# Optimization experiments

Hardware: AMD Instinct MI355X
Metric: run time of the kernel (lower is better)

Reference implementation:

```python
import jax, jax.numpy as jnp
import numpy as np
from jax import lax

B, C, H, W = 2, 128, 128, 128
Hs, Ws = 64, 64
DG, KK = 8, 9          # deformable groups, kernel positions (3x3)
CG = C // DG           # channels per deformable group = 16
COUT = C // 2          # dcn output channels = 64


def setup_inputs() -> dict:
    key = jax.random.key(0)
    ks = jax.random.split(key, 9)
    s = 0.05
    return {
        "feat_l": jax.random.normal(ks[0], (B, C, H, W), jnp.float32),
        "feat_s": jax.random.normal(ks[1], (B, C, Hs, Ws), jnp.float32),
        "fsm_w": jax.random.normal(ks[2], (C, C, 1, 1), jnp.float32) * s,
        "offset_w": jax.random.normal(ks[3], (C, 2 * C, 1, 1), jnp.float32) * s,
        "com_w": jax.random.normal(ks[4], (3 * DG * KK, C, 3, 3), jnp.float32) * s,
        "com_b": jax.random.normal(ks[5], (3 * DG * KK,), jnp.float32) * s,
        "dcn_w": jax.random.normal(ks[6], (COUT, C, 3, 3), jnp.float32) * s,
        "dcn_b": jax.random.normal(ks[7], (COUT,), jnp.float32) * s,
        "cat_w": jax.random.normal(ks[8], (C, COUT, 1, 1), jnp.float32) * s,
    }


def _conv(x, w, pad):
    return lax.conv_general_dilated(x, w, (1, 1), [(pad, pad), (pad, pad)],
                                    dimension_numbers=("NCHW", "OIHW", "NCHW"))


def _bilinear(feat_g, py, px):
    # feat_g: [B,DG,CG,H,W]; py/px: [B,DG,KK,H,W] fractional sample coords.
    Hf, Wf = feat_g.shape[-2], feat_g.shape[-1]
    y0 = jnp.floor(py)
    x0 = jnp.floor(px)
    ly = py - y0
    lx = px - x0
    y0i = y0.astype(jnp.int32)
    x0i = x0.astype(jnp.int32)
    flat = feat_g.reshape(B, DG, 1, CG, Hf * Wf)  # broadcast over KK

    def gather(yi, xi, wgt):
        valid = ((yi >= 0) & (yi < Hf) & (xi >= 0) & (xi < Wf)).astype(feat_g.dtype)
        idx = (jnp.clip(yi, 0, Hf - 1) * Wf + jnp.clip(xi, 0, Wf - 1))
        idx = idx.reshape(B, DG, KK, 1, H * W)
        v = jnp.take_along_axis(flat, idx, axis=-1)  # [B,DG,KK,CG,H*W]
        return v * (wgt * valid).reshape(B, DG, KK, 1, H * W)

    acc = (gather(y0i, x0i, (1 - ly) * (1 - lx))
           + gather(y0i, x0i + 1, (1 - ly) * lx)
           + gather(y0i + 1, x0i, ly * (1 - lx))
           + gather(y0i + 1, x0i + 1, ly * lx))
    return acc.reshape(B, DG, KK, CG, H, W)


def reference(feat_l, feat_s, fsm_w, offset_w, com_w, com_b, dcn_w, dcn_b, cat_w):
    # nearest-neighbor upsample of feat_s to feat_l's HxW (F.interpolate nearest)
    idx_h = (jnp.arange(H) * Hs) // H
    idx_w = (jnp.arange(W) * Ws) // W
    feat_up = feat_s[:, :, idx_h][:, :, :, idx_w]

    feat_arm = jax.nn.relu(_conv(feat_l, fsm_w, 0))                       # FSM (1x1 conv+relu)
    off_feat = jax.nn.relu(_conv(jnp.concatenate([feat_arm, feat_up * 2], axis=1), offset_w, 0))

    # DCNv2 pack: 3x3 conv -> (o1, o2, mask)
    om = _conv(off_feat, com_w, 1) + com_b[None, :, None, None]
    o1, o2, m = jnp.split(om, 3, axis=1)
    offset = jnp.concatenate([o1, o2], axis=1).reshape(B, DG, KK, 2, H, W)  # (y,x) per (g,pos)
    mask = jax.nn.sigmoid(m).reshape(B, DG, KK, H, W)

    # sampling coords: p + kernel offset + learned offset (stride=1, pad=1, dil=1)
    kyy = (jnp.arange(KK) // 3 - 1).astype(jnp.float32)
    kxx = (jnp.arange(KK) % 3 - 1).astype(jnp.float32)
    py = (jnp.arange(H, dtype=jnp.float32)[None, None, None, :, None]
          + kyy[None, None, :, None, None] + offset[:, :, :, 0])
    px = (jnp.arange(W, dtype=jnp.float32)[None, None, None, None, :]
          + kxx[None, None, :, None, None] + offset[:, :, :, 1])

    feat_g = feat_up.reshape(B, DG, CG, H, W)
    val = _bilinear(feat_g, py, px) * mask[:, :, :, None]  # [B,DG,KK,CG,H,W]

    w_r = dcn_w.reshape(COUT, DG, CG, KK)
    out = jnp.einsum('bgkchw,ogck->bohw', val, w_r) + dcn_b[None, :, None, None]
    feat_align = jax.nn.relu(out)

    return jax.nn.relu(_conv(feat_align, cat_w, 0)) + feat_arm
```

## Files before the change

kernel.cpp:

```cpp
#include <hip/hip_runtime.h>
#include <cstdint>
#include <cstddef>


typedef _Float16 f16x8 __attribute__((ext_vector_type(8)));
typedef _Float16 f16x4 __attribute__((ext_vector_type(4)));
typedef float    f32x4 __attribute__((ext_vector_type(4)));

__device__ __forceinline__ float relu_(float x) { return fmaxf(x, 0.f); }

template<int MODE, int CIN>
__global__ __launch_bounds__(256) void conv1x1_kernel(
    const float* __restrict__ in1, const float* __restrict__ in2,
    const float* __restrict__ Wm, float* __restrict__ out)
{
  constexpr int IN1C = (MODE == 2) ? 64 : 128;
  const int b  = blockIdx.y;
  const int p0 = blockIdx.x * 64;
  const int tid = threadIdx.x;
  const int tx = tid & 7;
  const int ty = tid >> 3;

  __shared__ float Xs[16][64];
  __shared__ float Wt[16][128];

  float acc[4][8];
#pragma unroll
  for (int i = 0; i < 4; ++i)
#pragma unroll
    for (int j = 0; j < 8; ++j) acc[i][j] = 0.f;

  const int cS  = tid >> 4;
  const int pxS = (tid & 15) * 4;
  const int ocS = (tid & 15) * 8;

  for (int cc = 0; cc < CIN; cc += 16) {
    __syncthreads();
    {
      int gc = cc + cS;
      float4 v;
      if (MODE == 1 && gc >= 128) {
        int sc = gc - 128;
        float t[4];
#pragma unroll
        for (int j = 0; j < 4; ++j) {
          int pp = p0 + pxS + j;
          int hh = pp >> 7, ww = pp & 127;
          t[j] = 2.f * in2[((size_t)(b * 128 + sc) << 12) + ((hh >> 1) << 6) + (ww >> 1)];
        }
        v = make_float4(t[0], t[1], t[2], t[3]);
      } else {
        v = *(const float4*)(in1 + ((size_t)(b * IN1C + gc) << 14) + p0 + pxS);
      }
      *(float4*)&Xs[cS][pxS] = v;
#pragma unroll
      for (int j = 0; j < 8; ++j)
        Wt[cS][ocS + j] = Wm[(ocS + j) * CIN + cc + cS];
    }
    __syncthreads();
#pragma unroll
    for (int c = 0; c < 16; ++c) {
      float4 wv = *(const float4*)&Wt[c][ty * 4];
      float4 x0 = *(const float4*)&Xs[c][tx * 8];
      float4 x1 = *(const float4*)&Xs[c][tx * 8 + 4];
      float xs[8] = {x0.x, x0.y, x0.z, x0.w, x1.x, x1.y, x1.z, x1.w};
      float wf[4] = {wv.x, wv.y, wv.z, wv.w};
#pragma unroll
      for (int i = 0; i < 4; ++i)
#pragma unroll
        for (int j = 0; j < 8; ++j)
          acc[i][j] = fmaf(wf[i], xs[j], acc[i][j]);
    }
  }

#pragma unroll
  for (int i = 0; i < 4; ++i) {
    int oc = ty * 4 + i;
    size_t base = ((size_t)(b * 128 + oc) << 14) + p0 + tx * 8;
    float r[8];
#pragma unroll
    for (int j = 0; j < 8; ++j) r[j] = relu_(acc[i][j]);
    if (MODE == 2) {
#pragma unroll
      for (int j = 0; j < 8; ++j) r[j] += in2[base + j];
    }
    *(float4*)(out + base)     = make_float4(r[0], r[1], r[2], r[3]);
    *(float4*)(out + base + 4) = make_float4(r[4], r[5], r[6], r[7]);
  }
}

__global__ __launch_bounds__(256) void t2h_kernel(
    const float* __restrict__ src, _Float16* __restrict__ dst, int HW)
{
  const int b  = blockIdx.z;
  const int c0 = blockIdx.y * 32;
  const int p0 = blockIdx.x * 32;
  const int tid = threadIdx.x;
  __shared__ float T[32][33];
  {
    int pxl = tid & 31, cy = tid >> 5;
#pragma unroll
    for (int j = 0; j < 4; ++j) {
      int c = cy + j * 8;
      T[c][pxl] = src[((size_t)(b * 128 + c0 + c)) * HW + p0 + pxl];
    }
  }
  __syncthreads();
  {
    int cq = tid & 7, pr = tid >> 3;
    f16x4 v;
#pragma unroll
    for (int e = 0; e < 4; ++e) v[e] = (_Float16)T[cq * 4 + e][pr];
    *(f16x4*)&dst[(((size_t)b * HW) + p0 + pr) * 128 + c0 + cq * 4] = v;
  }
}

__global__ __launch_bounds__(256) void wfA_kernel(
    const float* __restrict__ w, _Float16* __restrict__ Wf)
{
  int idx = blockIdx.x * 256 + threadIdx.x;
  int lane = idx & 63;
  int t = idx >> 6;
  int m = t & 7, q = t >> 3;
  int oc = m * 16 + (lane & 15);
  int c0 = q * 32 + (lane >> 4) * 8;
  f16x8 v;
#pragma unroll
  for (int j = 0; j < 8; ++j) v[j] = (_Float16)w[oc * 128 + c0 + j];
  ((f16x8*)Wf)[idx] = v;
}

__global__ __launch_bounds__(256) void wfB_kernel(
    const float* __restrict__ w, _Float16* __restrict__ Wf)
{
  int idx = blockIdx.x * 256 + threadIdx.x;
  int lane = idx & 63;
  int t = idx >> 6;
  int m = t & 7, q = t >> 3;
  int oc = m * 16 + (lane & 15);
  int c0 = q * 32 + (lane >> 4) * 8;
  float s = (q >= 4) ? 2.f : 1.f;
  f16x8 v;
#pragma unroll
  for (int j = 0; j < 8; ++j) v[j] = (_Float16)(w[oc * 256 + c0 + j] * s);
  ((f16x8*)Wf)[idx] = v;
}

__global__ __launch_bounds__(256) void wfP_kernel(
    const float* __restrict__ cw, _Float16* __restrict__ WfP)
{
  int idx = blockIdx.x * 256 + threadIdx.x;
  int lane = idx & 63;
  int t = idx >> 6;
  int m = t & 7;
  int t2 = t >> 3;
  int half = t2 & 1, q = t2 >> 1;
  int kk = q >> 2;
  int ic0 = (q & 3) * 32 + (lane >> 4) * 8;
  int oc = half * 128 + m * 16 + (lane & 15);
  f16x8 v;
#pragma unroll
  for (int j = 0; j < 8; ++j) {
    float x = (oc < 216) ? cw[((size_t)oc * 128 + ic0 + j) * 9 + kk] : 0.f;
    v[j] = (_Float16)x;
  }
  ((f16x8*)WfP)[idx] = v;
}

__global__ __launch_bounds__(256) void wf2_kernel(
    const float* __restrict__ dw, _Float16* __restrict__ Wf2)
{
  int idx = blockIdx.x * 256 + threadIdx.x;
  int lane = idx & 63;
  int t = idx >> 6;
  int m = t & 3, q = t >> 2;
  int oc = m * 16 + (lane & 15);
  f16x8 v;
#pragma unroll
  for (int j = 0; j < 8; ++j) {
    int rp = q * 32 + (lane >> 4) * 8 + j;
    int c = rp & 15, tt = rp >> 4;
    int g = tt / 9, k = tt % 9;
    v[j] = (_Float16)dw[((size_t)oc * 128 + g * 16 + c) * 9 + k];
  }
  ((f16x8*)Wf2)[idx] = v;
}

__global__ __launch_bounds__(256) void wfC_kernel(
    const float* __restrict__ w, _Float16* __restrict__ Wf)
{
  int idx = blockIdx.x * 256 + threadIdx.x;
  int lane = idx & 63;
  int t = idx >> 6;
  int m = t & 7, q = t >> 3;
  int oc = m * 16 + (lane & 15);
  int k0 = q * 32 + (lane >> 4) * 8;
  f16x8 v;
#pragma unroll
  for (int j = 0; j < 8; ++j) v[j] = (_Float16)w[oc * 64 + k0 + j];
  ((f16x8*)Wf)[idx] = v;
}

__global__ __launch_bounds__(256) void fsm_gemm_kernel(
    const _Float16* __restrict__ flTh, const _Float16* __restrict__ WfA,
    float* __restrict__ arm, _Float16* __restrict__ armh)
{
  const int b    = blockIdx.y;
  const int tid  = threadIdx.x;
  const int wv   = tid >> 6;
  const int lane = tid & 63;
  const int px0  = blockIdx.x * 64 + wv * 16;
  const int pxl  = px0 + (lane & 15);

  f32x4 acc[8];
#pragma unroll
  for (int m = 0; m < 8; ++m) acc[m] = (f32x4){0.f, 0.f, 0.f, 0.f};

  const f16x8* Bp = (const f16x8*)flTh + (((size_t)b << 14) + pxl) * 16 + (lane >> 4);
  const f16x8* Ap = (const f16x8*)WfA + lane;

#pragma unroll
  for (int q = 0; q < 4; ++q) {
    f16x8 bf = Bp[q * 4];
#pragma unroll
    for (int m = 0; m < 8; ++m)
      acc[m] = __builtin_amdgcn_mfma_f32_16x16x32_f16(Ap[(q * 8 + m) * 64], bf, acc[m], 0, 0, 0);
  }

  const int r0 = (lane >> 4) * 4;
#pragma unroll
  for (int m = 0; m < 8; ++m) {
    f16x4 h;
#pragma unroll
    for (int r = 0; r < 4; ++r) {
      float v = relu_(acc[m][r]);
      arm[((size_t)(b * 128 + m * 16 + r0 + r) << 14) + pxl] = v;
      h[r] = (_Float16)v;
    }
    *(f16x4*)&armh[(((size_t)b << 14) + pxl) * 128 + m * 16 + r0] = h;
  }
}

__global__ __launch_bounds__(256) void off_gemm_kernel(
    const _Float16* __restrict__ armh, const _Float16* __restrict__ fsTh,
    const _Float16* __restrict__ WfB, _Float16* __restrict__ offh)
{
  const int b    = blockIdx.y;
  const int tid  = threadIdx.x;
  const int wv   = tid >> 6;
  const int lane = tid & 63;
  const int px0  = blockIdx.x * 64 + wv * 16;
  const int pxl  = px0 + (lane & 15);
  const int h = pxl >> 7, w = pxl & 127;
  const int pup = ((h >> 1) << 6) + (w >> 1);

  f32x4 acc[8];
#pragma unroll
  for (int m = 0; m < 8; ++m) acc[m] = (f32x4){0.f, 0.f, 0.f, 0.f};

  const f16x8* BpA = (const f16x8*)armh + (((size_t)b << 14) + pxl) * 16 + (lane >> 4);
  const f16x8* BpU = (const f16x8*)fsTh + (((size_t)b << 12) + pup) * 16 + (lane >> 4);
  const f16x8* Ap  = (const f16x8*)WfB + lane;

#pragma unroll
  for (int q = 0; q < 8; ++q) {
    f16x8 bf = (q < 4) ? BpA[q * 4] : BpU[(q - 4) * 4];
#pragma unroll
    for (int m = 0; m < 8; ++m)
      acc[m] = __builtin_amdgcn_mfma_f32_16x16x32_f16(Ap[(q * 8 + m) * 64], bf, acc[m], 0, 0, 0);
  }

  const int r0 = (lane >> 4) * 4;
#pragma unroll
  for (int m = 0; m < 8; ++m) {
    f16x4 hh;
#pragma unroll
    for (int r = 0; r < 4; ++r) hh[r] = (_Float16)relu_(acc[m][r]);
    *(f16x4*)&offh[(((size_t)b << 14) + pxl) * 128 + m * 16 + r0] = hh;
  }
}

__global__ __launch_bounds__(256) void com_gemm_kernel(
    const _Float16* __restrict__ offh, const _Float16* __restrict__ WfP,
    const float* __restrict__ cb, float* __restrict__ om)
{
  const int b    = blockIdx.z;
  const int half = blockIdx.y;
  const int tid  = threadIdx.x;
  const int wv   = tid >> 6;
  const int lane = tid & 63;
  const int px0  = blockIdx.x * 64 + wv * 16;
  const int pxl  = px0 + (lane & 15);
  const int h = pxl >> 7, w = pxl & 127;

  __shared__ f16x8 As[512];

  f32x4 acc[8];
#pragma unroll
  for (int m = 0; m < 8; ++m) acc[m] = (f32x4){0.f, 0.f, 0.f, 0.f};

  const f16x8* Bbase = (const f16x8*)offh + ((size_t)b << 14) * 16 + (lane >> 4);
  const f16x8* Wp    = (const f16x8*)WfP + half * 512 + tid * 2;
  const f16x8 zero = {(_Float16)0.f, (_Float16)0.f, (_Float16)0.f, (_Float16)0.f,
                      (_Float16)0.f, (_Float16)0.f, (_Float16)0.f, (_Float16)0.f};

  f16x8 r0 = Wp[0];
  f16x8 r1 = Wp[1];

#pragma unroll 1
  for (int t = 0; t < 36; ++t) {
    __syncthreads();
    As[tid * 2]     = r0;
    As[tid * 2 + 1] = r1;
    __syncthreads();
    if (t < 35) {
      r0 = Wp[(t + 1) * 1024];
      r1 = Wp[(t + 1) * 1024 + 1];
    }
    const int kk = t >> 2, ic4 = t & 3;
    const int hh = h + kk / 3 - 1;
    const int ww = w + kk % 3 - 1;
    const bool valid = ((unsigned)hh < 128u) && ((unsigned)ww < 128u);
    const int ps = valid ? ((hh << 7) + ww) : 0;
    f16x8 bf = Bbase[(size_t)ps * 16 + ic4 * 4];
    bf = valid ? bf : zero;
#pragma unroll
    for (int m = 0; m < 8; ++m) {
      f16x8 af = As[m * 64 + lane];
      acc[m] = __builtin_amdgcn_mfma_f32_16x16x32_f16(af, bf, acc[m], 0, 0, 0);
    }
  }

  const int r0i = (lane >> 4) * 4;
#pragma unroll
  for (int m = 0; m < 8; ++m) {
#pragma unroll
    for (int r = 0; r < 4; ++r) {
      int oc = half * 128 + m * 16 + r0i + r;
      if (oc < 216)
        om[((size_t)(b * 216 + oc) << 14) + pxl] = acc[m][r] + cb[oc];
    }
  }
}

__global__ __launch_bounds__(256) void sample_kernel(
    const _Float16* __restrict__ fsTh, const float* __restrict__ om,
    _Float16* __restrict__ valh)
{
  const int idx = blockIdx.x * 256 + threadIdx.x;
  const int px = idx & 16383;
  const int t  = idx >> 14;
  const int k  = t % 9;
  const int g  = (t / 9) & 7;
  const int b  = t / 72;
  const int h = px >> 7, w = px & 127;

  const size_t omb = ((size_t)b * 216) << 14;
  const float offy = om[omb + ((size_t)(g * 18 + 2 * k) << 14) + px];
  const float offx = om[omb + ((size_t)(g * 18 + 2 * k + 1) << 14) + px];
  const float mraw = om[omb + ((size_t)(144 + g * 9 + k) << 14) + px];
  const float mv = 1.f / (1.f + __expf(-mraw));

  const float py  = (float)(h + k / 3 - 1) + offy;
  const float pxx = (float)(w + k % 3 - 1) + offx;
  const float y0f = floorf(py), x0f = floorf(pxx);
  const float ly = py - y0f, lx = pxx - x0f;
  const int y0 = (int)y0f, x0i = (int)x0f;
  const int y1 = y0 + 1, x1 = x0i + 1;

  const int y0c = min(max(y0, 0), 127), y1c = min(max(y1, 0), 127);
  const int x0c = min(max(x0i, 0), 127), x1c = min(max(x1, 0), 127);

  float w00 = (1.f - ly) * (1.f - lx) * mv;
  float w01 = (1.f - ly) * lx * mv;
  float w10 = ly * (1.f - lx) * mv;
  float w11 = ly * lx * mv;
  const bool vy0 = (unsigned)y0 < 128u, vy1 = (unsigned)y1 < 128u;
  const bool vx0 = (unsigned)x0i < 128u, vx1 = (unsigned)x1 < 128u;
  w00 = (vy0 && vx0) ? w00 : 0.f;
  w01 = (vy0 && vx1) ? w01 : 0.f;
  w10 = (vy1 && vx0) ? w10 : 0.f;
  w11 = (vy1 && vx1) ? w11 : 0.f;

  const _Float16* fb = fsTh + (((size_t)b << 12) << 7);
  const int a00 = ((((y0c >> 1) << 6) + (x0c >> 1)) << 7) + g * 16;
  const int a01 = ((((y0c >> 1) << 6) + (x1c >> 1)) << 7) + g * 16;
  const int a10 = ((((y1c >> 1) << 6) + (x0c >> 1)) << 7) + g * 16;
  const int a11 = ((((y1c >> 1) << 6) + (x1c >> 1)) << 7) + g * 16;

  f16x8 t00a = *(const f16x8*)(fb + a00), t00b = *(const f16x8*)(fb + a00 + 8);
  f16x8 t01a = *(const f16x8*)(fb + a01), t01b = *(const f16x8*)(fb + a01 + 8);
  f16x8 t10a = *(const f16x8*)(fb + a10), t10b = *(const f16x8*)(fb + a10 + 8);
  f16x8 t11a = *(const f16x8*)(fb + a11), t11b = *(const f16x8*)(fb + a11 + 8);

  f16x8 ov[2];
#pragma unroll
  for (int j = 0; j < 8; ++j) {
    ov[0][j] = (_Float16)(w00 * (float)t00a[j] + w01 * (float)t01a[j]
                        + w10 * (float)t10a[j] + w11 * (float)t11a[j]);
    ov[1][j] = (_Float16)(w00 * (float)t00b[j] + w01 * (float)t01b[j]
                        + w10 * (float)t10b[j] + w11 * (float)t11b[j]);
  }

  const int t9 = g * 9 + k;
  _Float16* dst = valh + (((size_t)(b * 36 + (t9 >> 1)) * 16384 + px) * 32 + (t9 & 1) * 16);
  ((f16x8*)dst)[0] = ov[0];
  ((f16x8*)dst)[1] = ov[1];
}

__global__ __launch_bounds__(256) void dcn_gemm_kernel(
    const _Float16* __restrict__ valh, const _Float16* __restrict__ Wf2,
    const float* __restrict__ db, _Float16* __restrict__ alh)
{
  const int b    = blockIdx.y;
  const int tid  = threadIdx.x;
  const int wv   = tid >> 6;
  const int lane = tid & 63;
  const int px0  = blockIdx.x * 32 + (wv >> 1) * 16;
  const int m0   = (wv & 1) * 2;

  f32x4 acc[2];
  acc[0] = (f32x4){0.f, 0.f, 0.f, 0.f};
  acc[1] = (f32x4){0.f, 0.f, 0.f, 0.f};

  const f16x8* Bp = (const f16x8*)valh
      + ((size_t)(b * 36) * 16384 + px0 + (lane & 15)) * 4 + (lane >> 4);
  const f16x8* Ap = (const f16x8*)Wf2 + m0 * 64 + lane;

#pragma unroll 2
  for (int q = 0; q < 36; ++q) {
    f16x8 bf = Bp[(size_t)q * 65536];
    const f16x8* ap = Ap + q * (4 * 64);
    f16x8 a0 = ap[0];
    f16x8 a1 = ap[64];
    acc[0] = __builtin_amdgcn_mfma_f32_16x16x32_f16(a0, bf, acc[0], 0, 0, 0);
    acc[1] = __builtin_amdgcn_mfma_f32_16x16x32_f16(a1, bf, acc[1], 0, 0, 0);
  }

  const int pxl = px0 + (lane & 15);
  const int r0  = (lane >> 4) * 4;
#pragma unroll
  for (int mm = 0; mm < 2; ++mm) {
    f16x4 hv;
#pragma unroll
    for (int r = 0; r < 4; ++r) {
      int oc = (m0 + mm) * 16 + r0 + r;
      hv[r] = (_Float16)relu_(acc[mm][r] + db[oc]);
    }
    *(f16x4*)&alh[(((size_t)b << 14) + pxl) * 64 + (m0 + mm) * 16 + r0] = hv;
  }
}

__global__ __launch_bounds__(256) void cat_gemm_kernel(
    const _Float16* __restrict__ alh, const _Float16* __restrict__ WfC,
    const float* __restrict__ arm, float* __restrict__ out)
{
  const int b    = blockIdx.y;
  const int tid  = threadIdx.x;
  const int wv   = tid >> 6;
  const int lane = tid & 63;
  const int px0  = blockIdx.x * 64 + wv * 16;
  const int pxl  = px0 + (lane & 15);

  f32x4 acc[8];
#pragma unroll
  for (int m = 0; m < 8; ++m) acc[m] = (f32x4){0.f, 0.f, 0.f, 0.f};

  const f16x8* Bp = (const f16x8*)alh + (((size_t)b << 14) + pxl) * 8 + (lane >> 4);
  const f16x8* Ap = (const f16x8*)WfC + lane;

#pragma unroll
  for (int q = 0; q < 2; ++q) {
    f16x8 bf = Bp[q * 4];
#pragma unroll
    for (int m = 0; m < 8; ++m)
      acc[m] = __builtin_amdgcn_mfma_f32_16x16x32_f16(Ap[(q * 8 + m) * 64], bf, acc[m], 0, 0, 0);
  }

  const int r0 = (lane >> 4) * 4;
#pragma unroll
  for (int m = 0; m < 8; ++m) {
#pragma unroll
    for (int r = 0; r < 4; ++r) {
      int oc = m * 16 + r0 + r;
      size_t a = ((size_t)(b * 128 + oc) << 14) + pxl;
      out[a] = relu_(acc[m][r]) + arm[a];
    }
  }
}

__global__ __launch_bounds__(256) void com_conv_kernel(
    const float* __restrict__ x, const float* __restrict__ cw,
    const float* __restrict__ cb, float* __restrict__ om)
{
  const int b    = blockIdx.z;
  const int ocg  = blockIdx.y;
  const int tile = blockIdx.x;
  const int th = (tile >> 2) * 32, tw = (tile & 3) * 32;
  const int tid = threadIdx.x;
  const int lw = (tid & 7) * 4;
  const int lh = tid >> 3;

  __shared__ float Xs[8 * 34 * 34];

  float acc[8][4];
#pragma unroll
  for (int a = 0; a < 8; ++a)
#pragma unroll
    for (int p = 0; p < 4; ++p) acc[a][p] = 0.f;

  for (int cc = 0; cc < 128; cc += 8) {
    __syncthreads();
    for (int idx = tid; idx < 8 * 1156; idx += 256) {
      int ic  = idx / 1156;
      int rem = idx - ic * 1156;
      int yy  = rem / 34;
      int xx  = rem - yy * 34;
      int gh = th + yy - 1, gw = tw + xx - 1;
      float v = 0.f;
      if ((unsigned)gh < 128u && (unsigned)gw < 128u)
        v = x[((size_t)(b * 128 + cc + ic) << 14) + (gh << 7) + gw];
      Xs[idx] = v;
    }
    __syncthreads();
#pragma unroll 1
    for (int ic = 0; ic < 8; ++ic) {
      float xr[3][6];
#pragma unroll
      for (int ky = 0; ky < 3; ++ky)
#pragma unroll
        for (int xx = 0; xx < 6; ++xx)
          xr[ky][xx] = Xs[ic * 1156 + (lh + ky) * 34 + lw + xx];
      const float* wp = cw + ((size_t)(ocg * 8) * 128 + (cc + ic)) * 9;
#pragma unroll
      for (int a = 0; a < 8; ++a) {
        const float* w9 = wp + a * 1152;
#pragma unroll
        for (int ky = 0; ky < 3; ++ky)
#pragma unroll
          for (int kx = 0; kx < 3; ++kx) {
            float wv = w9[ky * 3 + kx];
#pragma unroll
            for (int p = 0; p < 4; ++p)
              acc[a][p] = fmaf(wv, xr[ky][kx + p], acc[a][p]);
          }
      }
    }
  }

#pragma unroll
  for (int a = 0; a < 8; ++a) {
    int oc = ocg * 8 + a;
    float bv = cb[oc];
    float4 r = make_float4(acc[a][0] + bv, acc[a][1] + bv,
                           acc[a][2] + bv, acc[a][3] + bv);
    *(float4*)(om + ((size_t)(b * 216 + oc) << 14) + ((th + lh) << 7) + tw + lw) = r;
  }
}

__global__ __launch_bounds__(256) void wt_kernel(const float* __restrict__ dw,
                                                 float* __restrict__ wT)
{
  int idx = blockIdx.x * 256 + threadIdx.x;
  int o    = idx & 63;
  int rest = idx >> 6;
  int k    = rest % 9;
  int gc   = rest / 9;
  wT[idx] = dw[(o * 128 + gc) * 9 + k];
}

__global__ __launch_bounds__(256) void dcn_kernel(
    const float* __restrict__ fs, const float* __restrict__ om,
    const float* __restrict__ wT, const float* __restrict__ db,
    float* __restrict__ al)
{
  const int b   = blockIdx.y;
  const int p0  = blockIdx.x * 32;
  const int tid = threadIdx.x;
  const int px  = tid & 31;
  const int g   = tid >> 5;
  const int p = p0 + px;
  const int h = p >> 7, w = p & 127;

  float acc[64];
#pragma unroll
  for (int o = 0; o < 64; ++o) acc[o] = 0.f;

  const size_t omb = ((size_t)b * 216) << 14;
  const float* fsg = fs + (((size_t)(b * 128 + g * 16)) << 12);
  const float* wg  = wT + g * (16 * 9 * 64);

#pragma unroll 1
  for (int k = 0; k < 9; ++k) {
    float offy = om[omb + ((size_t)(g * 18 + 2 * k) << 14) + p];
    float offx = om[omb + ((size_t)(g * 18 + 2 * k + 1) << 14) + p];
    float mraw = om[omb + ((size_t)(144 + g * 9 + k) << 14) + p];
    float mv = 1.f / (1.f + __expf(-mraw));

    float py  = (float)(h + k / 3 - 1) + offy;
    float pxx = (float)(w + k % 3 - 1) + offx;
    float y0f = floorf(py), x0f = floorf(pxx);
    float ly = py - y0f, lx = pxx - x0f;
    int y0 = (int)y0f, x0i = (int)x0f;
    int y1 = y0 + 1, x1 = x0i + 1;

    int y0c = min(max(y0, 0), 127), y1c = min(max(y1, 0), 127);
    int x0c = min(max(x0i, 0), 127), x1c = min(max(x1, 0), 127);
    int ry0 = (y0c >> 1) << 6, ry1 = (y1c >> 1) << 6;
    int cx0 = x0c >> 1, cx1 = x1c >> 1;

    float w00 = (1.f - ly) * (1.f - lx) * mv;
    float w01 = (1.f - ly) * lx * mv;
    float w10 = ly * (1.f - lx) * mv;
    float w11 = ly * lx * mv;
    bool vy0 = (unsigned)y0 < 128u, vy1 = (unsigned)y1 < 128u;
    bool vx0 = (unsigned)x0i < 128u, vx1 = (unsigned)x1 < 128u;
    w00 = (vy0 && vx0) ? w00 : 0.f;
    w01 = (vy0 && vx1) ? w01 : 0.f;
    w10 = (vy1 && vx0) ? w10 : 0.f;
    w11 = (vy1 && vx1) ? w11 : 0.f;

#pragma unroll 1
    for (int c = 0; c < 16; ++c) {
      const float* fc = fsg + (c << 12);
      float v00 = fc[ry0 + cx0];
      float v01 = fc[ry0 + cx1];
      float v10 = fc[ry1 + cx0];
      float v11 = fc[ry1 + cx1];
      float v = w00 * v00 + w01 * v01 + w10 * v10 + w11 * v11;
      const float* wp = wg + (c * 9 + k) * 64;
#pragma unroll
      for (int oq = 0; oq < 16; ++oq) {
        float4 w4 = *(const float4*)(wp + oq * 4);
        acc[oq * 4 + 0] = fmaf(v, w4.x, acc[oq * 4 + 0]);
        acc[oq * 4 + 1] = fmaf(v, w4.y, acc[oq * 4 + 1]);
        acc[oq * 4 + 2] = fmaf(v, w4.z, acc[oq * 4 + 2]);
        acc[oq * 4 + 3] = fmaf(v, w4.w, acc[oq * 4 + 3]);
      }
    }
  }

  __shared__ float red[256][17];
  const int px2 = tid & 31;
  const int og  = tid >> 5;
#pragma unroll
  for (int r = 0; r < 4; ++r) {
    __syncthreads();
#pragma unroll
    for (int j = 0; j < 16; ++j) red[tid][j] = acc[r * 16 + j];
    __syncthreads();
#pragma unroll
    for (int jj = 0; jj < 2; ++jj) {
      int ol = og * 2 + jj;
      float s = 0.f;
#pragma unroll
      for (int gg = 0; gg < 8; ++gg) s += red[gg * 32 + px2][ol];
      int oc = r * 16 + ol;
      s += db[oc];
      al[((size_t)(b * 64 + oc) << 14) + p0 + px2] = fmaxf(s, 0.f);
    }
  }
}

extern "C" void kernel_launch(void* const* d_in, const int* in_sizes, int n_in,
                              void* d_out, int out_size, void* d_ws, size_t ws_size,
                              hipStream_t stream)
{
  const float* feat_l   = (const float*)d_in[0];
  const float* feat_s   = (const float*)d_in[1];
  const float* fsm_w    = (const float*)d_in[2];
  const float* offset_w = (const float*)d_in[3];
  const float* com_w    = (const float*)d_in[4];
  const float* com_b    = (const float*)d_in[5];
  const float* dcn_w    = (const float*)d_in[6];
  const float* dcn_b    = (const float*)d_in[7];
  const float* cat_w    = (const float*)d_in[8];
  float* out = (float*)d_out;
  float* ws  = (float*)d_ws;

  const size_t NEED = (size_t)(4194304 + 7077888 + 2097152 + 1048576 + 37748736) * 4;

  if (ws_size >= NEED) {
    float* arm      = ws;
    float* om       = ws + 4194304;
    _Float16* alh   = (_Float16*)(ws + 11272192);
    _Float16* Wf2   = (_Float16*)(ws + 12320768);
    _Float16* WfC   = (_Float16*)(ws + 12357632);
    _Float16* fsTh  = (_Float16*)(ws + 13369344);
    _Float16* flTh  = (_Float16*)(ws + 13893632);
    _Float16* armh  = (_Float16*)(ws + 15990784);
    _Float16* offh  = (_Float16*)(ws + 18087936);
    _Float16* valh  = (_Float16*)(ws + 20185088);
    _Float16* WfA   = (_Float16*)(ws + 39059456);
    _Float16* WfB   = (_Float16*)(ws + 39067648);
    _Float16* WfP   = (_Float16*)(ws + 39084032);

    hipLaunchKernelGGL(wfA_kernel, dim3(8), dim3(256), 0, stream, fsm_w, WfA);
    hipLaunchKernelGGL(wfB_kernel, dim3(16), dim3(256), 0, stream, offset_w, WfB);
    hipLaunchKernelGGL(wfP_kernel, dim3(144), dim3(256), 0, stream, com_w, WfP);
    hipLaunchKernelGGL(wf2_kernel, dim3(36), dim3(256), 0, stream, dcn_w, Wf2);
    hipLaunchKernelGGL(wfC_kernel, dim3(4), dim3(256), 0, stream, cat_w, WfC);
    hipLaunchKernelGGL(t2h_kernel, dim3(512, 4, 2), dim3(256), 0, stream,
                       feat_l, flTh, 16384);
    hipLaunchKernelGGL(t2h_kernel, dim3(128, 4, 2), dim3(256), 0, stream,
                       feat_s, fsTh, 4096);
    hipLaunchKernelGGL(fsm_gemm_kernel, dim3(256, 2), dim3(256), 0, stream,
                       flTh, WfA, arm, armh);
    hipLaunchKernelGGL(off_gemm_kernel, dim3(256, 2), dim3(256), 0, stream,
                       armh, fsTh, WfB, offh);
    hipLaunchKernelGGL(com_gemm_kernel, dim3(256, 2, 2), dim3(256), 0, stream,
                       offh, WfP, com_b, om);
    hipLaunchKernelGGL(sample_kernel, dim3(9216), dim3(256), 0, stream,
                       fsTh, om, valh);
    hipLaunchKernelGGL(dcn_gemm_kernel, dim3(512, 2), dim3(256), 0, stream,
                       valh, Wf2, dcn_b, alh);
    hipLaunchKernelGGL(cat_gemm_kernel, dim3(256, 2), dim3(256), 0, stream,
                       alh, WfC, arm, out);
  } else {
    float* arm = ws;
    float* off = ws + 4194304;
    float* om  = ws + 8388608;
    float* al  = ws + 15466496;
    float* wT  = ws + 17563648;

    hipLaunchKernelGGL(wt_kernel, dim3(288), dim3(256), 0, stream, dcn_w, wT);
    hipLaunchKernelGGL((conv1x1_kernel<0, 128>), dim3(256, 2), dim3(256), 0, stream,
                       feat_l, nullptr, fsm_w, arm);
    hipLaunchKernelGGL((conv1x1_kernel<1, 256>), dim3(256, 2), dim3(256), 0, stream,
                       arm, feat_s, offset_w, off);
    hipLaunchKernelGGL(com_conv_kernel, dim3(16, 27, 2), dim3(256), 0, stream,
                       off, com_w, com_b, om);
    hipLaunchKernelGGL(dcn_kernel, dim3(512, 2), dim3(256), 0, stream,
                       feat_s, om, wT, dcn_b, al);
    hipLaunchKernelGGL((conv1x1_kernel<2, 64>), dim3(256, 2), dim3(256), 0, stream,
                       al, arm, cat_w, out);
  }
}
```

Measured before the change: 225.6 us.

## Merge prep kernels, double-buffer com GEMM, vectorize sampling, widen dcn tiles

Folds the five weight-reformatting kernels into one launch and the two NCHW-to-NHWC half transposes into one. The com GEMM loop is unrolled by two so the next B-operand gather is prefetched while MFMAs run. The sampling kernel now handles four pixels per thread using float4 loads of offsets and mask. The dcn GEMM gives each wave all four output tiles over 16 pixels, so each B fragment is reused four times. The aims are less launch overhead and fewer redundant global loads, at the cost of more registers per thread and fewer blocks in the sampling and dcn kernels.

```diff
diff --git a/kernel.cpp b/kernel.cpp
--- a/kernel.cpp
+++ b/kernel.cpp
@@ -89,12 +89,18 @@
   }
 }
 
-__global__ __launch_bounds__(256) void t2h_kernel(
-    const float* __restrict__ src, _Float16* __restrict__ dst, int HW)
-{
+__global__ __launch_bounds__(256) void t2h2_kernel(
+    const float* __restrict__ fl, const float* __restrict__ fs,
+    _Float16* __restrict__ flTh, _Float16* __restrict__ fsTh)
+{
+  const int bx = blockIdx.x;
+  const float* src;
+  _Float16* dst;
+  int HW, p0;
+  if (bx < 512) { src = fl; dst = flTh; HW = 16384; p0 = bx * 32; }
+  else          { src = fs; dst = fsTh; HW = 4096;  p0 = (bx - 512) * 32; }
   const int b  = blockIdx.z;
   const int c0 = blockIdx.y * 32;
-  const int p0 = blockIdx.x * 32;
   const int tid = threadIdx.x;
   __shared__ float T[32][33];
   {
@@ -115,90 +121,82 @@
   }
 }
 
-__global__ __launch_bounds__(256) void wfA_kernel(
-    const float* __restrict__ w, _Float16* __restrict__ Wf)
-{
-  int idx = blockIdx.x * 256 + threadIdx.x;
-  int lane = idx & 63;
-  int t = idx >> 6;
-  int m = t & 7, q = t >> 3;
-  int oc = m * 16 + (lane & 15);
-  int c0 = q * 32 + (lane >> 4) * 8;
-  f16x8 v;
-#pragma unroll
-  for (int j = 0; j < 8; ++j) v[j] = (_Float16)w[oc * 128 + c0 + j];
-  ((f16x8*)Wf)[idx] = v;
-}
-
-__global__ __launch_bounds__(256) void wfB_kernel(
-    const float* __restrict__ w, _Float16* __restrict__ Wf)
-{
-  int idx = blockIdx.x * 256 + threadIdx.x;
-  int lane = idx & 63;
-  int t = idx >> 6;
-  int m = t & 7, q = t >> 3;
-  int oc = m * 16 + (lane & 15);
-  int c0 = q * 32 + (lane >> 4) * 8;
-  float s = (q >= 4) ? 2.f : 1.f;
-  f16x8 v;
-#pragma unroll
-  for (int j = 0; j < 8; ++j) v[j] = (_Float16)(w[oc * 256 + c0 + j] * s);
-  ((f16x8*)Wf)[idx] = v;
-}
-
-__global__ __launch_bounds__(256) void wfP_kernel(
-    const float* __restrict__ cw, _Float16* __restrict__ WfP)
-{
-  int idx = blockIdx.x * 256 + threadIdx.x;
-  int lane = idx & 63;
-  int t = idx >> 6;
-  int m = t & 7;
-  int t2 = t >> 3;
-  int half = t2 & 1, q = t2 >> 1;
-  int kk = q >> 2;
-  int ic0 = (q & 3) * 32 + (lane >> 4) * 8;
-  int oc = half * 128 + m * 16 + (lane & 15);
-  f16x8 v;
-#pragma unroll
-  for (int j = 0; j < 8; ++j) {
-    float x = (oc < 216) ? cw[((size_t)oc * 128 + ic0 + j) * 9 + kk] : 0.f;
-    v[j] = (_Float16)x;
-  }
-  ((f16x8*)WfP)[idx] = v;
-}
-
-__global__ __launch_bounds__(256) void wf2_kernel(
-    const float* __restrict__ dw, _Float16* __restrict__ Wf2)
-{
-  int idx = blockIdx.x * 256 + threadIdx.x;
-  int lane = idx & 63;
-  int t = idx >> 6;
-  int m = t & 3, q = t >> 2;
-  int oc = m * 16 + (lane & 15);
-  f16x8 v;
-#pragma unroll
-  for (int j = 0; j < 8; ++j) {
-    int rp = q * 32 + (lane >> 4) * 8 + j;
-    int c = rp & 15, tt = rp >> 4;
-    int g = tt / 9, k = tt % 9;
-    v[j] = (_Float16)dw[((size_t)oc * 128 + g * 16 + c) * 9 + k];
-  }
-  ((f16x8*)Wf2)[idx] = v;
-}
-
-__global__ __launch_bounds__(256) void wfC_kernel(
-    const float* __restrict__ w, _Float16* __restrict__ Wf)
-{
-  int idx = blockIdx.x * 256 + threadIdx.x;
-  int lane = idx & 63;
-  int t = idx >> 6;
-  int m = t & 7, q = t >> 3;
-  int oc = m * 16 + (lane & 15);
-  int k0 = q * 32 + (lane >> 4) * 8;
-  f16x8 v;
-#pragma unroll
-  for (int j = 0; j < 8; ++j) v[j] = (_Float16)w[oc * 64 + k0 + j];
-  ((f16x8*)Wf)[idx] = v;
+__global__ __launch_bounds__(256) void wfall_kernel(
+    const float* __restrict__ fsm_w, const float* __restrict__ offset_w,
+    const float* __restrict__ com_w, const float* __restrict__ dcn_w,
+    const float* __restrict__ cat_w,
+    _Float16* __restrict__ WfA, _Float16* __restrict__ WfB,
+    _Float16* __restrict__ WfP, _Float16* __restrict__ Wf2,
+    _Float16* __restrict__ WfC)
+{
+  const int bid = blockIdx.x;
+  if (bid < 8) {
+    int idx = bid * 256 + threadIdx.x;
+    int lane = idx & 63;
+    int t = idx >> 6;
+    int m = t & 7, q = t >> 3;
+    int oc = m * 16 + (lane & 15);
+    int c0 = q * 32 + (lane >> 4) * 8;
+    f16x8 v;
+#pragma unroll
+    for (int j = 0; j < 8; ++j) v[j] = (_Float16)fsm_w[oc * 128 + c0 + j];
+    ((f16x8*)WfA)[idx] = v;
+  } else if (bid < 24) {
+    int idx = (bid - 8) * 256 + threadIdx.x;
+    int lane = idx & 63;
+    int t = idx >> 6;
+    int m = t & 7, q = t >> 3;
+    int oc = m * 16 + (lane & 15);
+    int c0 = q * 32 + (lane >> 4) * 8;
+    float s = (q >= 4) ? 2.f : 1.f;
+    f16x8 v;
+#pragma unroll
+    for (int j = 0; j < 8; ++j) v[j] = (_Float16)(offset_w[oc * 256 + c0 + j] * s);
+    ((f16x8*)WfB)[idx] = v;
+  } else if (bid < 168) {
+    int idx = (bid - 24) * 256 + threadIdx.x;
+    int lane = idx & 63;
+    int t = idx >> 6;
+    int m = t & 7;
+    int t2 = t >> 3;
+    int half = t2 & 1, q = t2 >> 1;
+    int kk = q >> 2;
+    int ic0 = (q & 3) * 32 + (lane >> 4) * 8;
+    int oc = half * 128 + m * 16 + (lane & 15);
+    f16x8 v;
+#pragma unroll
+    for (int j = 0; j < 8; ++j) {
+      float x = (oc < 216) ? com_w[((size_t)oc * 128 + ic0 + j) * 9 + kk] : 0.f;
+      v[j] = (_Float16)x;
+    }
+    ((f16x8*)WfP)[idx] = v;
+  } else if (bid < 204) {
+    int idx = (bid - 168) * 256 + threadIdx.x;
+    int lane = idx & 63;
+    int t = idx >> 6;
+    int m = t & 3, q = t >> 2;
+    int oc = m * 16 + (lane & 15);
+    f16x8 v;
+#pragma unroll
+    for (int j = 0; j < 8; ++j) {
+      int rp = q * 32 + (lane >> 4) * 8 + j;
+      int c = rp & 15, tt = rp >> 4;
+      int g = tt / 9, k = tt % 9;
+      v[j] = (_Float16)dcn_w[((size_t)oc * 128 + g * 16 + c) * 9 + k];
+    }
+    ((f16x8*)Wf2)[idx] = v;
+  } else {
+    int idx = (bid - 204) * 256 + threadIdx.x;
+    int lane = idx & 63;
+    int t = idx >> 6;
+    int m = t & 7, q = t >> 3;
+    int oc = m * 16 + (lane & 15);
+    int k0 = q * 32 + (lane >> 4) * 8;
+    f16x8 v;
+#pragma unroll
+    for (int j = 0; j < 8; ++j) v[j] = (_Float16)cat_w[oc * 64 + k0 + j];
+    ((f16x8*)WfC)[idx] = v;
+  }
 }
 
 __global__ __launch_bounds__(256) void fsm_gemm_kernel(
@@ -287,9 +285,8 @@
   const int b    = blockIdx.z;
   const int half = blockIdx.y;
   const int tid  = threadIdx.x;
-  const int wv   = tid >> 6;
   const int lane = tid & 63;
-  const int px0  = blockIdx.x * 64 + wv * 16;
+  const int px0  = blockIdx.x * 64 + (tid >> 6) * 16;
   const int pxl  = px0 + (lane & 15);
   const int h = pxl >> 7, w = pxl & 127;
 
@@ -304,30 +301,43 @@
   const f16x8 zero = {(_Float16)0.f, (_Float16)0.f, (_Float16)0.f, (_Float16)0.f,
                       (_Float16)0.f, (_Float16)0.f, (_Float16)0.f, (_Float16)0.f};
 
-  f16x8 r0 = Wp[0];
-  f16x8 r1 = Wp[1];
-
-#pragma unroll 1
-  for (int t = 0; t < 36; ++t) {
-    __syncthreads();
-    As[tid * 2]     = r0;
-    As[tid * 2 + 1] = r1;
-    __syncthreads();
-    if (t < 35) {
-      r0 = Wp[(t + 1) * 1024];
-      r1 = Wp[(t + 1) * 1024 + 1];
-    }
+  auto loadB = [&](int t) -> f16x8 {
     const int kk = t >> 2, ic4 = t & 3;
     const int hh = h + kk / 3 - 1;
     const int ww = w + kk % 3 - 1;
     const bool valid = ((unsigned)hh < 128u) && ((unsigned)ww < 128u);
     const int ps = valid ? ((hh << 7) + ww) : 0;
     f16x8 bf = Bbase[(size_t)ps * 16 + ic4 * 4];
-    bf = valid ? bf : zero;
-#pragma unroll
-    for (int m = 0; m < 8; ++m) {
-      f16x8 af = As[m * 64 + lane];
-      acc[m] = __builtin_amdgcn_mfma_f32_16x16x32_f16(af, bf, acc[m], 0, 0, 0);
+    return valid ? bf : zero;
+  };
+
+  f16x8 rA0 = Wp[0], rA1 = Wp[1];
+  f16x8 bfA = loadB(0), bfB = loadB(1);
+
+#pragma unroll 1
+  for (int tt = 0; tt < 18; ++tt) {
+    const int t0 = tt * 2;
+    __syncthreads();
+    As[tid * 2] = rA0; As[tid * 2 + 1] = rA1;
+    __syncthreads();
+    rA0 = Wp[(t0 + 1) * 1024]; rA1 = Wp[(t0 + 1) * 1024 + 1];
+    {
+      f16x8 bu = bfA;
+      if (t0 + 2 < 36) bfA = loadB(t0 + 2);
+#pragma unroll
+      for (int m = 0; m < 8; ++m)
+        acc[m] = __builtin_amdgcn_mfma_f32_16x16x32_f16(As[m * 64 + lane], bu, acc[m], 0, 0, 0);
+    }
+    __syncthreads();
+    As[tid * 2] = rA0; As[tid * 2 + 1] = rA1;
+    __syncthreads();
+    if (t0 + 2 < 36) { rA0 = Wp[(t0 + 2) * 1024]; rA1 = Wp[(t0 + 2) * 1024 + 1]; }
+    {
+      f16x8 bu = bfB;
+      if (t0 + 3 < 36) bfB = loadB(t0 + 3);
+#pragma unroll
+      for (int m = 0; m < 8; ++m)
+        acc[m] = __builtin_amdgcn_mfma_f32_16x16x32_f16(As[m * 64 + lane], bu, acc[m], 0, 0, 0);
     }
   }
 
@@ -348,64 +358,75 @@
     _Float16* __restrict__ valh)
 {
   const int idx = blockIdx.x * 256 + threadIdx.x;
-  const int px = idx & 16383;
-  const int t  = idx >> 14;
+  const int px4 = (idx & 4095) << 2;
+  const int t  = idx >> 12;
   const int k  = t % 9;
   const int g  = (t / 9) & 7;
   const int b  = t / 72;
-  const int h = px >> 7, w = px & 127;
 
   const size_t omb = ((size_t)b * 216) << 14;
-  const float offy = om[omb + ((size_t)(g * 18 + 2 * k) << 14) + px];
-  const float offx = om[omb + ((size_t)(g * 18 + 2 * k + 1) << 14) + px];
-  const float mraw = om[omb + ((size_t)(144 + g * 9 + k) << 14) + px];
-  const float mv = 1.f / (1.f + __expf(-mraw));
-
-  const float py  = (float)(h + k / 3 - 1) + offy;
-  const float pxx = (float)(w + k % 3 - 1) + offx;
-  const float y0f = floorf(py), x0f = floorf(pxx);
-  const float ly = py - y0f, lx = pxx - x0f;
-  const int y0 = (int)y0f, x0i = (int)x0f;
-  const int y1 = y0 + 1, x1 = x0i + 1;
-
-  const int y0c = min(max(y0, 0), 127), y1c = min(max(y1, 0), 127);
-  const int x0c = min(max(x0i, 0), 127), x1c = min(max(x1, 0), 127);
-
-  float w00 = (1.f - ly) * (1.f - lx) * mv;
-  float w01 = (1.f - ly) * lx * mv;
-  float w10 = ly * (1.f - lx) * mv;
-  float w11 = ly * lx * mv;
-  const bool vy0 = (unsigned)y0 < 128u, vy1 = (unsigned)y1 < 128u;
-  const bool vx0 = (unsigned)x0i < 128u, vx1 = (unsigned)x1 < 128u;
-  w00 = (vy0 && vx0) ? w00 : 0.f;
-  w01 = (vy0 && vx1) ? w01 : 0.f;
-  w10 = (vy1 && vx0) ? w10 : 0.f;
-  w11 = (vy1 && vx1) ? w11 : 0.f;
-
-  const _Float16* fb = fsTh + (((size_t)b << 12) << 7);
-  const int a00 = ((((y0c >> 1) << 6) + (x0c >> 1)) << 7) + g * 16;
-  const int a01 = ((((y0c >> 1) << 6) + (x1c >> 1)) << 7) + g * 16;
-  const int a10 = ((((y1c >> 1) << 6) + (x0c >> 1)) << 7) + g * 16;
-  const int a11 = ((((y1c >> 1) << 6) + (x1c >> 1)) << 7) + g * 16;
-
-  f16x8 t00a = *(const f16x8*)(fb + a00), t00b = *(const f16x8*)(fb + a00 + 8);
-  f16x8 t01a = *(const f16x8*)(fb + a01), t01b = *(const f16x8*)(fb + a01 + 8);
-  f16x8 t10a = *(const f16x8*)(fb + a10), t10b = *(const f16x8*)(fb + a10 + 8);
-  f16x8 t11a = *(const f16x8*)(fb + a11), t11b = *(const f16x8*)(fb + a11 + 8);
-
-  f16x8 ov[2];
-#pragma unroll
-  for (int j = 0; j < 8; ++j) {
-    ov[0][j] = (_Float16)(w00 * (float)t00a[j] + w01 * (float)t01a[j]
+  const float4 oy4 = *(const float4*)(om + omb + ((size_t)(g * 18 + 2 * k) << 14) + px4);
+  const float4 ox4 = *(const float4*)(om + omb + ((size_t)(g * 18 + 2 * k + 1) << 14) + px4);
+  const float4 mr4 = *(const float4*)(om + omb + ((size_t)(144 + g * 9 + k) << 14) + px4);
+  const float oys[4] = {oy4.x, oy4.y, oy4.z, oy4.w};
+  const float oxs[4] = {ox4.x, ox4.y, ox4.z, ox4.w};
+  const float mrs[4] = {mr4.x, mr4.y, mr4.z, mr4.w};
+
+  const _Float16* fb = fsTh + ((size_t)b << 19);
+  const int t9 = g * 9 + k;
+  _Float16* dstb = valh + (((size_t)(b * 36 + (t9 >> 1)) * 16384 + px4) * 32 + (t9 & 1) * 16);
+
+  const int kdy = k / 3 - 1, kdx = k % 3 - 1;
+  const int h = px4 >> 7, w0 = px4 & 127;
+  const int gbase = g * 16;
+
+#pragma unroll
+  for (int i = 0; i < 4; ++i) {
+    const float mv = 1.f / (1.f + __expf(-mrs[i]));
+    const float py  = (float)(h + kdy) + oys[i];
+    const float pxx = (float)(w0 + i + kdx) + oxs[i];
+    const float y0f = floorf(py), x0f = floorf(pxx);
+    const float ly = py - y0f, lx = pxx - x0f;
+    const int y0 = (int)y0f, x0i = (int)x0f;
+    const int y1 = y0 + 1, x1 = x0i + 1;
+
+    const int y0c = min(max(y0, 0), 127), y1c = min(max(y1, 0), 127);
+    const int x0c = min(max(x0i, 0), 127), x1c = min(max(x1, 0), 127);
+
+    float w00 = (1.f - ly) * (1.f - lx) * mv;
+    float w01 = (1.f - ly) * lx * mv;
+    float w10 = ly * (1.f - lx) * mv;
+    float w11 = ly * lx * mv;
+    const bool vy0 = (unsigned)y0 < 128u, vy1 = (unsigned)y1 < 128u;
+    const bool vx0 = (unsigned)x0i < 128u, vx1 = (unsigned)x1 < 128u;
+    w00 = (vy0 && vx0) ? w00 : 0.f;
+    w01 = (vy0 && vx1) ? w01 : 0.f;
+    w10 = (vy1 && vx0) ? w10 : 0.f;
+    w11 = (vy1 && vx1) ? w11 : 0.f;
+
+    const int a00 = ((((y0c >> 1) << 6) + (x0c >> 1)) << 7) + gbase;
+    const int a01 = ((((y0c >> 1) << 6) + (x1c >> 1)) << 7) + gbase;
+    const int a10 = ((((y1c >> 1) << 6) + (x0c >> 1)) << 7) + gbase;
+    const int a11 = ((((y1c >> 1) << 6) + (x1c >> 1)) << 7) + gbase;
+
+    f16x8 t00a = *(const f16x8*)(fb + a00), t00b = *(const f16x8*)(fb + a00 + 8);
+    f16x8 t01a = *(const f16x8*)(fb + a01), t01b = *(const f16x8*)(fb + a01 + 8);
+    f16x8 t10a = *(const f16x8*)(fb + a10), t10b = *(const f16x8*)(fb + a10 + 8);
+    f16x8 t11a = *(const f16x8*)(fb + a11), t11b = *(const f16x8*)(fb + a11 + 8);
+
+    f16x8 ov0, ov1;
+#pragma unroll
+    for (int j = 0; j < 8; ++j) {
+      ov0[j] = (_Float16)(w00 * (float)t00a[j] + w01 * (float)t01a[j]
                         + w10 * (float)t10a[j] + w11 * (float)t11a[j]);
-    ov[1][j] = (_Float16)(w00 * (float)t00b[j] + w01 * (float)t01b[j]
+      ov1[j] = (_Float16)(w00 * (float)t00b[j] + w01 * (float)t01b[j]
                         + w10 * (float)t10b[j] + w11 * (float)t11b[j]);
-  }
-
-  const int t9 = g * 9 + k;
-  _Float16* dst = valh + (((size_t)(b * 36 + (t9 >> 1)) * 16384 + px) * 32 + (t9 & 1) * 16);
-  ((f16x8*)dst)[0] = ov[0];
-  ((f16x8*)dst)[1] = ov[1];
+    }
+
+    _Float16* dst = dstb + i * 32;
+    ((f16x8*)dst)[0] = ov0;
+    ((f16x8*)dst)[1] = ov1;
+  }
 }
 
 __global__ __launch_bounds__(256) void dcn_gemm_kernel(
@@ -416,38 +437,36 @@
   const int tid  = threadIdx.x;
   const int wv   = tid >> 6;
   const int lane = tid & 63;
-  const int px0  = blockIdx.x * 32 + (wv >> 1) * 16;
-  const int m0   = (wv & 1) * 2;
-
-  f32x4 acc[2];
-  acc[0] = (f32x4){0.f, 0.f, 0.f, 0.f};
-  acc[1] = (f32x4){0.f, 0.f, 0.f, 0.f};
+  const int px0  = blockIdx.x * 64 + wv * 16;
+
+  f32x4 acc[4];
+#pragma unroll
+  for (int m = 0; m < 4; ++m) acc[m] = (f32x4){0.f, 0.f, 0.f, 0.f};
 
   const f16x8* Bp = (const f16x8*)valh
       + ((size_t)(b * 36) * 16384 + px0 + (lane & 15)) * 4 + (lane >> 4);
-  const f16x8* Ap = (const f16x8*)Wf2 + m0 * 64 + lane;
+  const f16x8* Ap = (const f16x8*)Wf2 + lane;
 
 #pragma unroll 2
   for (int q = 0; q < 36; ++q) {
     f16x8 bf = Bp[(size_t)q * 65536];
-    const f16x8* ap = Ap + q * (4 * 64);
-    f16x8 a0 = ap[0];
-    f16x8 a1 = ap[64];
-    acc[0] = __builtin_amdgcn_mfma_f32_16x16x32_f16(a0, bf, acc[0], 0, 0, 0);
-    acc[1] = __builtin_amdgcn_mfma_f32_16x16x32_f16(a1, bf, acc[1], 0, 0, 0);
+    const f16x8* ap = Ap + q * 256;
+#pragma unroll
+    for (int m = 0; m < 4; ++m)
+      acc[m] = __builtin_amdgcn_mfma_f32_16x16x32_f16(ap[m * 64], bf, acc[m], 0, 0, 0);
   }
 
   const int pxl = px0 + (lane & 15);
   const int r0  = (lane >> 4) * 4;
 #pragma unroll
-  for (int mm = 0; mm < 2; ++mm) {
+  for (int m = 0; m < 4; ++m) {
     f16x4 hv;
 #pragma unroll
     for (int r = 0; r < 4; ++r) {
-      int oc = (m0 + mm) * 16 + r0 + r;
-      hv[r] = (_Float16)relu_(acc[mm][r] + db[oc]);
-    }
-    *(f16x4*)&alh[(((size_t)b << 14) + pxl) * 64 + (m0 + mm) * 16 + r0] = hv;
+      int oc = m * 16 + r0 + r;
+      hv[r] = (_Float16)relu_(acc[m][r] + db[oc]);
+    }
+    *(f16x4*)&alh[(((size_t)b << 14) + pxl) * 64 + m * 16 + r0] = hv;
   }
 }
 
@@ -695,24 +714,19 @@
     _Float16* WfB   = (_Float16*)(ws + 39067648);
     _Float16* WfP   = (_Float16*)(ws + 39084032);
 
-    hipLaunchKernelGGL(wfA_kernel, dim3(8), dim3(256), 0, stream, fsm_w, WfA);
-    hipLaunchKernelGGL(wfB_kernel, dim3(16), dim3(256), 0, stream, offset_w, WfB);
-    hipLaunchKernelGGL(wfP_kernel, dim3(144), dim3(256), 0, stream, com_w, WfP);
-    hipLaunchKernelGGL(wf2_kernel, dim3(36), dim3(256), 0, stream, dcn_w, Wf2);
-    hipLaunchKernelGGL(wfC_kernel, dim3(4), dim3(256), 0, stream, cat_w, WfC);
-    hipLaunchKernelGGL(t2h_kernel, dim3(512, 4, 2), dim3(256), 0, stream,
-                       feat_l, flTh, 16384);
-    hipLaunchKernelGGL(t2h_kernel, dim3(128, 4, 2), dim3(256), 0, stream,
-                       feat_s, fsTh, 4096);
+    hipLaunchKernelGGL(wfall_kernel, dim3(208), dim3(256), 0, stream,
+                       fsm_w, offset_w, com_w, dcn_w, cat_w, WfA, WfB, WfP, Wf2, WfC);
+    hipLaunchKernelGGL(t2h2_kernel, dim3(640, 4, 2), dim3(256), 0, stream,
+                       feat_l, feat_s, flTh, fsTh);
     hipLaunchKernelGGL(fsm_gemm_kernel, dim3(256, 2), dim3(256), 0, stream,
                        flTh, WfA, arm, armh);
     hipLaunchKernelGGL(off_gemm_kernel, dim3(256, 2), dim3(256), 0, stream,
                        armh, fsTh, WfB, offh);
     hipLaunchKernelGGL(com_gemm_kernel, dim3(256, 2, 2), dim3(256), 0, stream,
                        offh, WfP, com_b, om);
-    hipLaunchKernelGGL(sample_kernel, dim3(9216), dim3(256), 0, stream,
+    hipLaunchKernelGGL(sample_kernel, dim3(2304), dim3(256), 0, stream,
                        fsTh, om, valh);
-    hipLaunchKernelGGL(dcn_gemm_kernel, dim3(512, 2), dim3(256), 0, stream,
+    hipLaunchKernelGGL(dcn_gemm_kernel, dim3(256, 2), dim3(256), 0, stream,
                        valh, Wf2, dcn_b, alh);
     hipLaunchKernelGGL(cat_gemm_kernel, dim3(256, 2), dim3(256), 0, stream,
                        alh, WfC, arm, out);
```

After: 225.6 us. No clear change (-0.0%).
